# Kernel tuning notes

Measured on AMD Instinct MI355X. Metric: run time of the kernel, lower is better.

Reference implementation:

```python
import jax, jax.numpy as jnp
import numpy as np

N = 65536      # total nodes
B = 512        # graphs (equal-sized)
NPER = N // B  # 128 nodes per graph
E = 655360     # edges
F_IN = 128
K = 32         # sort-pool k
OUT = 27


def _gcn(x, row, col, dinv, W, b):
    # PyG GCNConv with added self-loops and symmetric normalization:
    xw = x @ W                                   # [N, F_out]
    coef = dinv[row] * dinv[col]                 # [E]
    agg = jax.ops.segment_sum(xw[row] * coef[:, None], col, num_segments=N)
    return agg + (dinv * dinv)[:, None] * xw + b  # self-loop term + bias


def _conv1d(x, w, b, stride):
    # x: [B, C_in, L], w: [C_out, C_in, K]
    out = jax.lax.conv_general_dilated(x, w, (stride,), 'VALID',
                                       dimension_numbers=('NCH', 'OIH', 'NCH'))
    return out + b[None, :, None]


def setup_inputs() -> dict:
    key = jax.random.key(0)
    ks = jax.random.split(key, 16)
    x = jax.random.normal(ks[0], (N, F_IN), dtype=jnp.float32)
    edge_index = jax.random.randint(ks[1], (2, E), 0, N, dtype=jnp.int32)
    batch = jnp.repeat(jnp.arange(B, dtype=jnp.int32), NPER)

    def lin(k, fi, fo):
        return jax.random.normal(k, (fi, fo), dtype=jnp.float32) / np.sqrt(fi)

    W1, b1 = lin(ks[2], F_IN, 128), jnp.zeros((128,), jnp.float32)
    W2, b2 = lin(ks[3], 128, 64), jnp.zeros((64,), jnp.float32)
    W3, b3 = lin(ks[4], 64, 32), jnp.zeros((32,), jnp.float32)
    W4, b4 = lin(ks[5], 32, 32), jnp.zeros((32,), jnp.float32)
    conv5_w = jax.random.normal(ks[6], (16, 1, 256), jnp.float32) / np.sqrt(256)
    conv5_b = jnp.zeros((16,), jnp.float32)
    conv6_w = jax.random.normal(ks[7], (32, 16, 5), jnp.float32) / np.sqrt(16 * 5)
    conv6_b = jnp.zeros((32,), jnp.float32)
    dense_w = lin(ks[8], 384, OUT)
    dense_b = jnp.zeros((OUT,), jnp.float32)
    return dict(x=x, edge_index=edge_index, batch=batch,
                W1=W1, b1=b1, W2=W2, b2=b2, W3=W3, b3=b3, W4=W4, b4=b4,
                conv5_w=conv5_w, conv5_b=conv5_b, conv6_w=conv6_w, conv6_b=conv6_b,
                dense_w=dense_w, dense_b=dense_b)


def reference(x, edge_index, batch, W1, b1, W2, b2, W3, b3, W4, b4,
              conv5_w, conv5_b, conv6_w, conv6_b, dense_w, dense_b):
    row, col = edge_index[0], edge_index[1]
    deg = jax.ops.segment_sum(jnp.ones((E,), x.dtype), col, num_segments=N) + 1.0
    dinv = jax.lax.rsqrt(deg)

    x1 = jnp.tanh(_gcn(x, row, col, dinv, W1, b1))
    x2 = jnp.tanh(_gcn(x1, row, col, dinv, W2, b2))
    x3 = jnp.tanh(_gcn(x2, row, col, dinv, W3, b3))
    x4 = jnp.tanh(_gcn(x3, row, col, dinv, W4, b4))
    h = jnp.concatenate([x1, x2, x3, x4], axis=-1)   # [N, 256]

    # SortAggregation: sort nodes within each graph by last channel (desc), take top-k.
    hg = h.reshape(B, NPER, 256)
    idx = jnp.argsort(-hg[:, :, -1], axis=1)[:, :K]                 # [B, K]
    pooled = jnp.take_along_axis(hg, idx[:, :, None], axis=1)       # [B, K, 256]
    top_k_indices = idx + (jnp.arange(B, dtype=idx.dtype) * NPER)[:, None]

    z = pooled.reshape(B, 1, K * 256)                # [B, 1, 8192]
    z = jax.nn.relu(_conv1d(z, conv5_w, conv5_b, 256))  # [B, 16, 32]
    z = jax.lax.reduce_window(z, -jnp.inf, jax.lax.max,
                              (1, 1, 2), (1, 1, 2), 'VALID')        # [B, 16, 16]
    z = jax.nn.relu(_conv1d(z, conv6_w, conv6_b, 1))  # [B, 32, 12]
    z = z.reshape(B, -1)                              # [B, 384]
    out = z @ dense_w + dense_b                       # [B, 27]
    return out, top_k_indices
```

## Files before the change

kernel.cpp:

```cpp
#include <hip/hip_runtime.h>
#include <math.h>

#define N_NODES 65536
#define N_EDGES 655360
#define N_GRAPHS 512
#define NPERG 128
#define KTOP 32
#define NOUT 27
#define OUT0_SIZE (N_GRAPHS * NOUT)
#define EPS 64

typedef unsigned int uint32;
typedef unsigned short u16;
typedef unsigned char u8;
typedef __attribute__((ext_vector_type(8))) short bf16x8;
typedef __attribute__((ext_vector_type(4))) float f32x4;
typedef __attribute__((ext_vector_type(2))) float f32x2;

__device__ __forceinline__ float blo(uint32 u) { return __uint_as_float(u << 16); }
__device__ __forceinline__ float bhi(uint32 u) { return __uint_as_float(u & 0xffff0000u); }
__device__ __forceinline__ u16 f2b(float f) {
    uint32 u = __float_as_uint(f);
    u += 0x7fffu + ((u >> 16) & 1u);
    return (u16)(u >> 16);
}
__device__ __forceinline__ uint32 pk(float a, float b) {
    return (uint32)f2b(a) | ((uint32)f2b(b) << 16);
}
__device__ __forceinline__ f32x2 fp8lo(uint32 u) { return __builtin_amdgcn_cvt_pk_f32_fp8((int)u, false); }
__device__ __forceinline__ f32x2 fp8hi(uint32 u) { return __builtin_amdgcn_cvt_pk_f32_fp8((int)u, true); }
__device__ __forceinline__ u8 f2fp8(float v) {
    return (u8)(__builtin_amdgcn_cvt_pk_fp8_f32(v, v, 0, false) & 0xff);
}


__global__ __launch_bounds__(256) void zero_kernel(int* __restrict__ cur) {
    cur[blockIdx.x * 256 + threadIdx.x] = 0;
}


template<int FI, int FO>
__device__ __forceinline__ void pack_w(const float* __restrict__ W, uint4* __restrict__ pw,
                                       int base, int nb) {
    constexpr int KC = FI / 8;
    for (int q = (blockIdx.x - base) * 256 + threadIdx.x; q < FO * KC; q += nb * 256) {
        int n = q % FO, c = q / FO;
        const float* wp = W + (size_t)(c * 8) * FO + n;
        uint4 v;
        v.x = pk(wp[0],            wp[(size_t)FO]);
        v.y = pk(wp[2*(size_t)FO], wp[3*(size_t)FO]);
        v.z = pk(wp[4*(size_t)FO], wp[5*(size_t)FO]);
        v.w = pk(wp[6*(size_t)FO], wp[7*(size_t)FO]);
        pw[n * KC + c] = v;
    }
}

__global__ __launch_bounds__(256) void prep_w(const float* __restrict__ W1, const float* __restrict__ W2,
                                              const float* __restrict__ W3, const float* __restrict__ W4,
                                              uint4* __restrict__ pw1, uint4* __restrict__ pw2,
                                              uint4* __restrict__ pw3, uint4* __restrict__ pw4) {
    int b = blockIdx.x;
    if (b < 8)       pack_w<128, 128>(W1, pw1, 0, 8);
    else if (b < 12) pack_w<128, 64>(W2, pw2, 8, 4);
    else if (b < 13) pack_w<64, 32>(W3, pw3, 12, 1);
    else             pack_w<32, 32>(W4, pw4, 13, 1);
}


__global__ __launch_bounds__(256) void fill_kernel(const int* __restrict__ erow, const int* __restrict__ ecol,
                                                   int* __restrict__ cur, u16* __restrict__ ep) {
    int e = blockIdx.x * 256 + threadIdx.x;
    int r = erow[e], d = ecol[e];
    int slot = atomicAdd(&cur[d], 1);
    if (slot < EPS) ep[(d << 6) + slot] = (u16)r;
}


__global__ __launch_bounds__(256) void dinv_kernel(const int* __restrict__ cur, float* __restrict__ dinv) {
    int i = blockIdx.x * 256 + threadIdx.x;
    dinv[i] = rsqrtf((float)cur[i] + 1.0f);
}


template<int FI, int FO>
__device__ __forceinline__ void stage_Bp(const uint4* __restrict__ pw, uint4* __restrict__ Bs) {
    constexpr int KC = FI / 8, SA = KC + 1;
    for (int q = threadIdx.x; q < FO * KC; q += 256) {
        int n = q / KC, c = q % KC;
        Bs[n * SA + c] = pw[q];
    }
}

template<int FI, int FO, bool OUT_FP8>
__device__ __forceinline__ void mfma_store(uint4* __restrict__ As, const uint4* __restrict__ Bs,
                                           uint4* __restrict__ Y, size_t rowbase,
                                           const float* __restrict__ ds) {
    constexpr int KC = FI / 8, SA = KC + 1;
    constexpr int NTILE = FO / 16;
    constexpr int CW = (NTILE >= 4) ? 4 : NTILE;
    constexpr int NTW = NTILE / CW;
    constexpr int RW = 4 / CW;
    constexpr int RS = 2 / RW;
    constexpr int KSTEPS = FI / 32;
    int t = threadIdx.x;
    int w = t >> 6, L = t & 63;
    int quad = L >> 4, m = L & 15;
    int cw = w % CW, rw = w / CW;

    const bf16x8* Asv = (const bf16x8*)As;
    const bf16x8* Bsv = (const bf16x8*)Bs;

    f32x4 acc[RS][NTW];
#pragma unroll
    for (int i = 0; i < RS; i++)
#pragma unroll
        for (int j = 0; j < NTW; j++) acc[i][j] = (f32x4)0.f;

#pragma unroll
    for (int ks = 0; ks < KSTEPS; ks++) {
        int kc = ks * 4 + quad;
        bf16x8 bfr[NTW];
#pragma unroll
        for (int j = 0; j < NTW; j++) {
            int n = (cw * NTW + j) * 16 + m;
            bfr[j] = Bsv[n * SA + kc];
        }
#pragma unroll
        for (int i = 0; i < RS; i++) {
            int r = (rw * RS + i) * 16 + m;
            bf16x8 afr = Asv[r * SA + kc];
#pragma unroll
            for (int j = 0; j < NTW; j++)
                acc[i][j] = __builtin_amdgcn_mfma_f32_16x16x32_bf16(afr, bfr[j], acc[i][j], 0, 0, 0);
        }
    }
    __syncthreads();

    if constexpr (OUT_FP8) {
        u8* outs = (u8*)As;
#pragma unroll
        for (int i = 0; i < RS; i++) {
            int rb = (rw * RS + i) * 16 + quad * 4;
#pragma unroll
            for (int j = 0; j < NTW; j++) {
                int cc = (cw * NTW + j) * 16 + m;
#pragma unroll
                for (int g2 = 0; g2 < 4; g2++)
                    outs[(rb + g2) * FO + cc] = f2fp8(acc[i][j][g2] * ds[rb + g2]);
            }
        }
    } else {
        u16* outs = (u16*)As;
#pragma unroll
        for (int i = 0; i < RS; i++) {
            int rb = (rw * RS + i) * 16 + quad * 4;
#pragma unroll
            for (int j = 0; j < NTW; j++) {
                int cc = (cw * NTW + j) * 16 + m;
#pragma unroll
                for (int g2 = 0; g2 < 4; g2++)
                    outs[(rb + g2) * FO + cc] = f2b(acc[i][j][g2] * ds[rb + g2]);
            }
        }
    }
    __syncthreads();
    constexpr int NU4 = OUT_FP8 ? (32 * FO / 16) : (32 * FO / 8);
    for (int q = t; q < NU4; q += 256)
        Y[rowbase * (NU4 / 32) + q] = ((const uint4*)As)[q];
}


__global__ __launch_bounds__(256) void gemm1_kernel(const float* __restrict__ x,
                                                    const uint4* __restrict__ pw1,
                                                    const float* __restrict__ dinv,
                                                    uint4* __restrict__ xw1) {
    constexpr int KC = 16, SA = 17;
    __shared__ __align__(16) uint4 As[32 * SA];
    __shared__ __align__(16) uint4 Bs[128 * SA];
    __shared__ float ds[32];
    int t = threadIdx.x;
    stage_Bp<128, 128>(pw1, Bs);
    size_t rowbase = (size_t)blockIdx.x * 32;
    if (t < 32) ds[t] = dinv[rowbase + t];
    for (int q = t; q < 32 * KC; q += 256) {
        int r = q / KC, c = q % KC;
        const float* xp = x + (rowbase + r) * 128 + c * 8;
        float4 v0 = *(const float4*)xp;
        float4 v1 = *(const float4*)(xp + 4);
        uint4 u;
        u.x = pk(v0.x, v0.y); u.y = pk(v0.z, v0.w);
        u.z = pk(v1.x, v1.y); u.w = pk(v1.z, v1.w);
        As[r * SA + c] = u;
    }
    __syncthreads();
    mfma_store<128, 128, true>(As, Bs, xw1, rowbase, ds);
}


template<int F>
__device__ __forceinline__ void agg_node_fp8(const uint32* __restrict__ xin1,
                                             const u16* __restrict__ ep,
                                             int n, int c4, int deg, float dn,
                                             const float* __restrict__ bias,
                                             float& r0, float& r1, float& r2, float& r3) {
    constexpr int L4 = F / 4;
    const u16* epp = ep + (n << 6);
    float a0=0.f,a1=0.f,a2=0.f,a3=0.f,b0=0.f,b1=0.f,b2=0.f,b3=0.f;
    float c0=0.f,c1=0.f,c2=0.f,c3=0.f,d0=0.f,d1=0.f,d2=0.f,d3=0.f;
    int full = deg >> 3; if (full > EPS / 8) full = EPS / 8;
    for (int b = 0; b < full; b++) {
        uint4 e8 = *(const uint4*)(epp + b * 8);
        uint32 q0=e8.x&0xffffu, q1=e8.x>>16, q2=e8.y&0xffffu, q3=e8.y>>16;
        uint32 q4=e8.z&0xffffu, q5=e8.z>>16, q6=e8.w&0xffffu, q7=e8.w>>16;
        uint32 g0=xin1[(size_t)q0*L4+c4], g1=xin1[(size_t)q1*L4+c4];
        uint32 g2=xin1[(size_t)q2*L4+c4], g3=xin1[(size_t)q3*L4+c4];
        uint32 g4=xin1[(size_t)q4*L4+c4], g5=xin1[(size_t)q5*L4+c4];
        uint32 g6=xin1[(size_t)q6*L4+c4], g7=xin1[(size_t)q7*L4+c4];
        f32x2 l, h;
        l=fp8lo(g0); h=fp8hi(g0); a0+=l.x; a1+=l.y; a2+=h.x; a3+=h.y;
        l=fp8lo(g1); h=fp8hi(g1); b0+=l.x; b1+=l.y; b2+=h.x; b3+=h.y;
        l=fp8lo(g2); h=fp8hi(g2); c0+=l.x; c1+=l.y; c2+=h.x; c3+=h.y;
        l=fp8lo(g3); h=fp8hi(g3); d0+=l.x; d1+=l.y; d2+=h.x; d3+=h.y;
        l=fp8lo(g4); h=fp8hi(g4); a0+=l.x; a1+=l.y; a2+=h.x; a3+=h.y;
        l=fp8lo(g5); h=fp8hi(g5); b0+=l.x; b1+=l.y; b2+=h.x; b3+=h.y;
        l=fp8lo(g6); h=fp8hi(g6); c0+=l.x; c1+=l.y; c2+=h.x; c3+=h.y;
        l=fp8lo(g7); h=fp8hi(g7); d0+=l.x; d1+=l.y; d2+=h.x; d3+=h.y;
    }
    int rem = (full == EPS / 8) ? 0 : (deg & 7);
    if (rem) {
        uint4 e8 = *(const uint4*)(epp + full * 8);
        uint32 q0=e8.x&0xffffu, q1=e8.x>>16, q2=e8.y&0xffffu, q3=e8.y>>16;
        uint32 q4=e8.z&0xffffu, q5=e8.z>>16, q6=e8.w&0xffffu, q7=e8.w>>16;
        uint32 g0=xin1[(size_t)q0*L4+c4], g1=xin1[(size_t)q1*L4+c4];
        uint32 g2=xin1[(size_t)q2*L4+c4], g3=xin1[(size_t)q3*L4+c4];
        uint32 g4=xin1[(size_t)q4*L4+c4], g5=xin1[(size_t)q5*L4+c4];
        uint32 g6=xin1[(size_t)q6*L4+c4], g7=xin1[(size_t)q7*L4+c4];
        g0 = (rem > 0) ? g0 : 0u; g1 = (rem > 1) ? g1 : 0u;
        g2 = (rem > 2) ? g2 : 0u; g3 = (rem > 3) ? g3 : 0u;
        g4 = (rem > 4) ? g4 : 0u; g5 = (rem > 5) ? g5 : 0u;
        g6 = (rem > 6) ? g6 : 0u; g7 = (rem > 7) ? g7 : 0u;
        f32x2 l, h;
        l=fp8lo(g0); h=fp8hi(g0); a0+=l.x; a1+=l.y; a2+=h.x; a3+=h.y;
        l=fp8lo(g1); h=fp8hi(g1); b0+=l.x; b1+=l.y; b2+=h.x; b3+=h.y;
        l=fp8lo(g2); h=fp8hi(g2); c0+=l.x; c1+=l.y; c2+=h.x; c3+=h.y;
        l=fp8lo(g3); h=fp8hi(g3); d0+=l.x; d1+=l.y; d2+=h.x; d3+=h.y;
        l=fp8lo(g4); h=fp8hi(g4); a0+=l.x; a1+=l.y; a2+=h.x; a3+=h.y;
        l=fp8lo(g5); h=fp8hi(g5); b0+=l.x; b1+=l.y; b2+=h.x; b3+=h.y;
        l=fp8lo(g6); h=fp8hi(g6); c0+=l.x; c1+=l.y; c2+=h.x; c3+=h.y;
        l=fp8lo(g7); h=fp8hi(g7); d0+=l.x; d1+=l.y; d2+=h.x; d3+=h.y;
    }
    uint32 sv = xin1[(size_t)n * L4 + c4];
    f32x2 sl = fp8lo(sv), sh = fp8hi(sv);
    r0 = dn * ((a0+b0+c0+d0) + sl.x) + bias[4*c4+0];
    r1 = dn * ((a1+b1+c1+d1) + sl.y) + bias[4*c4+1];
    r2 = dn * ((a2+b2+c2+d2) + sh.x) + bias[4*c4+2];
    r3 = dn * ((a3+b3+c3+d3) + sh.y) + bias[4*c4+3];
}

template<int F>
__device__ __forceinline__ void agg_node_bf16(const uint2* __restrict__ xin2,
                                              const u16* __restrict__ ep,
                                              int n, int c4, int deg, float dn,
                                              const float* __restrict__ bias,
                                              float& r0, float& r1, float& r2, float& r3) {
    constexpr int L4 = F / 4;
    const u16* epp = ep + (n << 6);
    float a0=0.f,a1=0.f,a2=0.f,a3=0.f,b0=0.f,b1=0.f,b2=0.f,b3=0.f;
    float c0=0.f,c1=0.f,c2=0.f,c3=0.f,d0=0.f,d1=0.f,d2=0.f,d3=0.f;
    int full = deg >> 3; if (full > EPS / 8) full = EPS / 8;
    for (int b = 0; b < full; b++) {
        uint4 e8 = *(const uint4*)(epp + b * 8);
        uint32 q0=e8.x&0xffffu, q1=e8.x>>16, q2=e8.y&0xffffu, q3=e8.y>>16;
        uint32 q4=e8.z&0xffffu, q5=e8.z>>16, q6=e8.w&0xffffu, q7=e8.w>>16;
        uint2 g0=xin2[(size_t)q0*L4+c4], g1=xin2[(size_t)q1*L4+c4];
        uint2 g2=xin2[(size_t)q2*L4+c4], g3=xin2[(size_t)q3*L4+c4];
        uint2 g4=xin2[(size_t)q4*L4+c4], g5=xin2[(size_t)q5*L4+c4];
        uint2 g6=xin2[(size_t)q6*L4+c4], g7=xin2[(size_t)q7*L4+c4];
        a0+=blo(g0.x); a1+=bhi(g0.x); a2+=blo(g0.y); a3+=bhi(g0.y);
        b0+=blo(g1.x); b1+=bhi(g1.x); b2+=blo(g1.y); b3+=bhi(g1.y);
        c0+=blo(g2.x); c1+=bhi(g2.x); c2+=blo(g2.y); c3+=bhi(g2.y);
        d0+=blo(g3.x); d1+=bhi(g3.x); d2+=blo(g3.y); d3+=bhi(g3.y);
        a0+=blo(g4.x); a1+=bhi(g4.x); a2+=blo(g4.y); a3+=bhi(g4.y);
        b0+=blo(g5.x); b1+=bhi(g5.x); b2+=blo(g5.y); b3+=bhi(g5.y);
        c0+=blo(g6.x); c1+=bhi(g6.x); c2+=blo(g6.y); c3+=bhi(g6.y);
        d0+=blo(g7.x); d1+=bhi(g7.x); d2+=blo(g7.y); d3+=bhi(g7.y);
    }
    int rem = (full == EPS / 8) ? 0 : (deg & 7);
    if (rem) {
        uint4 e8 = *(const uint4*)(epp + full * 8);
        uint32 q0=e8.x&0xffffu, q1=e8.x>>16, q2=e8.y&0xffffu, q3=e8.y>>16;
        uint32 q4=e8.z&0xffffu, q5=e8.z>>16, q6=e8.w&0xffffu, q7=e8.w>>16;
        uint2 g0=xin2[(size_t)q0*L4+c4], g1=xin2[(size_t)q1*L4+c4];
        uint2 g2=xin2[(size_t)q2*L4+c4], g3=xin2[(size_t)q3*L4+c4];
        uint2 g4=xin2[(size_t)q4*L4+c4], g5=xin2[(size_t)q5*L4+c4];
        uint2 g6=xin2[(size_t)q6*L4+c4], g7=xin2[(size_t)q7*L4+c4];
        g0.x=(rem>0)?g0.x:0u; g0.y=(rem>0)?g0.y:0u;
        g1.x=(rem>1)?g1.x:0u; g1.y=(rem>1)?g1.y:0u;
        g2.x=(rem>2)?g2.x:0u; g2.y=(rem>2)?g2.y:0u;
        g3.x=(rem>3)?g3.x:0u; g3.y=(rem>3)?g3.y:0u;
        g4.x=(rem>4)?g4.x:0u; g4.y=(rem>4)?g4.y:0u;
        g5.x=(rem>5)?g5.x:0u; g5.y=(rem>5)?g5.y:0u;
        g6.x=(rem>6)?g6.x:0u; g6.y=(rem>6)?g6.y:0u;
        g7.x=(rem>7)?g7.x:0u; g7.y=(rem>7)?g7.y:0u;
        a0+=blo(g0.x); a1+=bhi(g0.x); a2+=blo(g0.y); a3+=bhi(g0.y);
        b0+=blo(g1.x); b1+=bhi(g1.x); b2+=blo(g1.y); b3+=bhi(g1.y);
        c0+=blo(g2.x); c1+=bhi(g2.x); c2+=blo(g2.y); c3+=bhi(g2.y);
        d0+=blo(g3.x); d1+=bhi(g3.x); d2+=blo(g3.y); d3+=bhi(g3.y);
        a0+=blo(g4.x); a1+=bhi(g4.x); a2+=blo(g4.y); a3+=bhi(g4.y);
        b0+=blo(g5.x); b1+=bhi(g5.x); b2+=blo(g5.y); b3+=bhi(g5.y);
        c0+=blo(g6.x); c1+=bhi(g6.x); c2+=blo(g6.y); c3+=bhi(g6.y);
        d0+=blo(g7.x); d1+=bhi(g7.x); d2+=blo(g7.y); d3+=bhi(g7.y);
    }
    uint2 sv = xin2[(size_t)n * L4 + c4];
    r0 = dn * ((a0+b0+c0+d0) + blo(sv.x)) + bias[4*c4+0];
    r1 = dn * ((a1+b1+c1+d1) + bhi(sv.x)) + bias[4*c4+1];
    r2 = dn * ((a2+b2+c2+d2) + blo(sv.y)) + bias[4*c4+2];
    r3 = dn * ((a3+b3+c3+d3) + bhi(sv.y)) + bias[4*c4+3];
}


template<int F, int FO, bool IN_FP8>
__global__ __launch_bounds__(256, 6) void agg_gemm(const uint32* __restrict__ xin,
                                                   const int* __restrict__ cur,
                                                   const u16* __restrict__ ep,
                                                   const float* __restrict__ dinv,
                                                   const float* __restrict__ bias,
                                                   const uint4* __restrict__ pw,
                                                   uint32* __restrict__ hc, int co2,
                                                   uint4* __restrict__ xout) {
    constexpr int KC = F / 8, SA = KC + 1;
    constexpr int L4 = F / 4;
    constexpr int NPP = 256 / L4;
    __shared__ __align__(16) uint4 As[32 * SA];
    __shared__ __align__(16) uint4 Bs[FO * SA];
    __shared__ float ds[32];
    int t = threadIdx.x;
    int rowbase = blockIdx.x * 32;
    stage_Bp<F, FO>(pw, Bs);
    if (t < 32) ds[t] = dinv[rowbase + t];
    __syncthreads();

    uint2* As2 = (uint2*)As;
    uint2* hc2 = (uint2*)hc;
    int c4 = t % L4;
    int nsub = t / L4;
#pragma unroll
    for (int pass = 0; pass < 32 / NPP; pass++) {
        int nl = pass * NPP + nsub;
        int n = rowbase + nl;
        int deg = cur[n];
        float dn = ds[nl];
        float r0, r1, r2, r3;
        if constexpr (IN_FP8)
            agg_node_fp8<F>(xin, ep, n, c4, deg, dn, bias, r0, r1, r2, r3);
        else
            agg_node_bf16<F>((const uint2*)xin, ep, n, c4, deg, dn, bias, r0, r1, r2, r3);
        uint2 pr;
        pr.x = pk(tanhf(r0), tanhf(r1));
        pr.y = pk(tanhf(r2), tanhf(r3));
        hc2[(size_t)n * 64 + co2 + c4] = pr;
        As2[nl * (SA * 2) + c4] = pr;
    }
    __syncthreads();
    mfma_store<F, FO, false>(As, Bs, xout, (size_t)rowbase, ds);
}


__global__ __launch_bounds__(256) void agg_last(const uint32* __restrict__ xin,
                                                const int* __restrict__ cur,
                                                const u16* __restrict__ ep,
                                                const float* __restrict__ dinv,
                                                const float* __restrict__ b4,
                                                uint32* __restrict__ hc) {
    int t = threadIdx.x;
    int c4 = t & 7, nsub = t >> 3;
    int n = blockIdx.x * 32 + nsub;
    int deg = cur[n];
    float dn = dinv[n];
    float r0, r1, r2, r3;
    agg_node_bf16<32>((const uint2*)xin, ep, n, c4, deg, dn, b4, r0, r1, r2, r3);
    uint2 pr;
    pr.x = pk(tanhf(r0), tanhf(r1));
    pr.y = pk(tanhf(r2), tanhf(r3));
    ((uint2*)hc)[(size_t)n * 64 + 56 + c4] = pr;
}


__global__ __launch_bounds__(256) void final_kernel(const uint32* __restrict__ hc,
                                                    const float* __restrict__ w5, const float* __restrict__ b5,
                                                    const float* __restrict__ w6, const float* __restrict__ b6,
                                                    const float* __restrict__ dw, const float* __restrict__ db,
                                                    float* __restrict__ out) {
    __shared__ float skey[128];
    __shared__ int   sidx[128];
    __shared__ uint32 ph[32 * 133];
    __shared__ float w5s[4096];
    __shared__ float z5[16 * 33];
    __shared__ float ms[16 * 17];
    __shared__ float z6[384];
    int g = blockIdx.x, t = threadIdx.x;

    for (int q = t; q < 4096; q += 256) w5s[q] = w5[q];
    if (t < 128) { skey[t] = bhi(hc[(size_t)(g * NPERG + t) * 128 + 127]); sidx[t] = t; }
    __syncthreads();

    for (int sz = 2; sz <= 128; sz <<= 1) {
        for (int stride = sz >> 1; stride > 0; stride >>= 1) {
            if (t < 64) {
                int i = ((t & ~(stride - 1)) << 1) | (t & (stride - 1));
                int j = i | stride;
                float ki = skey[i], kj = skey[j];
                int ii = sidx[i], ij = sidx[j];
                bool desc = ((i & sz) == 0);
                bool ibef = (ki > kj) || (ki == kj && ii < ij);
                if (desc != ibef) { skey[i] = kj; skey[j] = ki; sidx[i] = ij; sidx[j] = ii; }
            }
            __syncthreads();
        }
    }

    if (t < KTOP) out[OUT0_SIZE + g * KTOP + t] = (float)(g * NPERG + sidx[t]);

    {
        const uint4* hcv = (const uint4*)hc;
        int rsub = t >> 5, cell = t & 31;
#pragma unroll
        for (int p = 0; p < 4; p++) {
            int r2 = p * 8 + rsub;
            int node = g * NPERG + sidx[r2];
            uint4 v = hcv[(size_t)node * 32 + cell];
            uint32* dst = &ph[r2 * 133 + cell * 4];
            dst[0] = v.x; dst[1] = v.y; dst[2] = v.z; dst[3] = v.w;
        }
    }
    __syncthreads();

    {
        int o = t >> 5, l = t & 31;
        float a0 = 0.f, a1 = 0.f;
#pragma unroll 4
        for (int j2 = 0; j2 < 128; j2++) {
            uint32 u = ph[l * 133 + j2];
            float p0 = blo(u), p1 = bhi(u);
            a0 += p0 * w5s[o * 256 + 2 * j2]       + p1 * w5s[o * 256 + 2 * j2 + 1];
            a1 += p0 * w5s[(o + 8) * 256 + 2 * j2] + p1 * w5s[(o + 8) * 256 + 2 * j2 + 1];
        }
        z5[o * 33 + l]       = fmaxf(a0 + b5[o], 0.f);
        z5[(o + 8) * 33 + l] = fmaxf(a1 + b5[o + 8], 0.f);
    }
    __syncthreads();

    {
        int o = t >> 4, p = t & 15;
        ms[o * 17 + p] = fmaxf(z5[o * 33 + 2 * p], z5[o * 33 + 2 * p + 1]);
    }
    __syncthreads();

    for (int q = t; q < 384; q += 256) {
        int o2 = q / 12, tt = q % 12;
        float a = b6[o2];
        for (int o = 0; o < 16; o++) {
#pragma unroll
            for (int k = 0; k < 5; k++)
                a += w6[(o2 * 16 + o) * 5 + k] * ms[o * 17 + tt + k];
        }
        z6[q] = fmaxf(a, 0.f);
    }
    __syncthreads();

    if (t < NOUT) {
        float a = db[t];
        for (int i = 0; i < 384; i++) a += z6[i] * dw[i * NOUT + t];
        out[g * NOUT + t] = a;
    }
}


extern "C" void kernel_launch(void* const* d_in, const int* in_sizes, int n_in,
                              void* d_out, int out_size, void* d_ws, size_t ws_size,
                              hipStream_t stream) {
    const float* x    = (const float*)d_in[0];
    const int*   edge = (const int*)d_in[1];
    const int*   erow = edge;
    const int*   ecol = edge + N_EDGES;
    const float* W1 = (const float*)d_in[3];  const float* b1 = (const float*)d_in[4];
    const float* W2 = (const float*)d_in[5];  const float* b2 = (const float*)d_in[6];
    const float* W3 = (const float*)d_in[7];  const float* b3 = (const float*)d_in[8];
    const float* W4 = (const float*)d_in[9];  const float* b4 = (const float*)d_in[10];
    const float* w5 = (const float*)d_in[11]; const float* b5 = (const float*)d_in[12];
    const float* w6 = (const float*)d_in[13]; const float* b6 = (const float*)d_in[14];
    const float* dw = (const float*)d_in[15]; const float* db = (const float*)d_in[16];
    float* out = (float*)d_out;

    char* wsb = (char*)d_ws;
    size_t off = 0;
    auto alloc = [&](size_t bytes) -> void* {
        void* p = wsb + off;
        off = (off + bytes + 255) & ~(size_t)255;
        return p;
    };
    int*    cur  = (int*)   alloc((size_t)N_NODES * 4);
    float*  dinv = (float*) alloc((size_t)N_NODES * 4);
    u16*    ep   = (u16*)   alloc((size_t)N_NODES * EPS * 2);
    uint32* xwA  = (uint32*)alloc((size_t)N_NODES * 32 * 4);
    uint32* xwB  = (uint32*)alloc((size_t)N_NODES * 32 * 4);
    uint32* hc   = (uint32*)alloc((size_t)N_NODES * 128 * 4);
    uint4*  pw1  = (uint4*) alloc(2048 * 16);
    uint4*  pw2  = (uint4*) alloc(1024 * 16);
    uint4*  pw3  = (uint4*) alloc(256 * 16);
    uint4*  pw4  = (uint4*) alloc(128 * 16);
    (void)ws_size; (void)in_sizes; (void)n_in; (void)out_size;

    zero_kernel<<<N_NODES / 256, 256, 0, stream>>>(cur);
    prep_w<<<14, 256, 0, stream>>>(W1, W2, W3, W4, pw1, pw2, pw3, pw4);
    fill_kernel<<<N_EDGES / 256, 256, 0, stream>>>(erow, ecol, cur, ep);
    dinv_kernel<<<N_NODES / 256, 256, 0, stream>>>(cur, dinv);
    gemm1_kernel<<<N_NODES / 32, 256, 0, stream>>>(x, pw1, dinv, (uint4*)xwA);
    agg_gemm<128, 64, true><<<N_NODES / 32, 256, 0, stream>>>(xwA, cur, ep, dinv, b1, pw2, hc, 0, (uint4*)xwB);
    agg_gemm<64, 32, false><<<N_NODES / 32, 256, 0, stream>>>(xwB, cur, ep, dinv, b2, pw3, hc, 32, (uint4*)xwA);
    agg_gemm<32, 32, false><<<N_NODES / 32, 256, 0, stream>>>(xwA, cur, ep, dinv, b3, pw4, hc, 48, (uint4*)xwB);
    agg_last<<<N_NODES / 32, 256, 0, stream>>>(xwB, cur, ep, dinv, b4, hc);
    final_kernel<<<N_GRAPHS, 256, 0, stream>>>(hc, w5, b5, w6, b6, dw, db, out);
}
```

Before: 246.4 us.

## Unroll neighbor gather to fixed 32 edges with masking and store layer-2 input as fp8

Merges the fp8 and bf16 aggregation helpers into one template. The new helper always issues 32 masked gathers up front, so many loads are in flight together instead of running a variable-length loop of 8. Edges beyond 32 go through a scalar tail loop. Layer 1's GEMM output is now written in fp8, so layer 2 reads its gathered features as fp8, halving that gather's bytes at some precision cost. Launch bounds drop from 6 to 4 waves per SIMD, giving more registers in exchange for lower occupancy, and low-degree nodes now issue wasted masked loads to node 0.

```diff
diff --git a/kernel.cpp b/kernel.cpp
--- a/kernel.cpp
+++ b/kernel.cpp
@@ -197,130 +197,86 @@
 }
 
 
-template<int F>
-__device__ __forceinline__ void agg_node_fp8(const uint32* __restrict__ xin1,
-                                             const u16* __restrict__ ep,
-                                             int n, int c4, int deg, float dn,
-                                             const float* __restrict__ bias,
-                                             float& r0, float& r1, float& r2, float& r3) {
+template<int F, bool FP8>
+__device__ __forceinline__ void agg_node(const void* __restrict__ xin,
+                                         const u16* __restrict__ ep,
+                                         int n, int c4, int deg, float dn,
+                                         const float* __restrict__ bias,
+                                         float& r0, float& r1, float& r2, float& r3) {
     constexpr int L4 = F / 4;
+    const uint32* x1 = (const uint32*)xin;
+    const uint2*  x2 = (const uint2*)xin;
     const u16* epp = ep + (n << 6);
-    float a0=0.f,a1=0.f,a2=0.f,a3=0.f,b0=0.f,b1=0.f,b2=0.f,b3=0.f;
-    float c0=0.f,c1=0.f,c2=0.f,c3=0.f,d0=0.f,d1=0.f,d2=0.f,d3=0.f;
-    int full = deg >> 3; if (full > EPS / 8) full = EPS / 8;
-    for (int b = 0; b < full; b++) {
-        uint4 e8 = *(const uint4*)(epp + b * 8);
-        uint32 q0=e8.x&0xffffu, q1=e8.x>>16, q2=e8.y&0xffffu, q3=e8.y>>16;
-        uint32 q4=e8.z&0xffffu, q5=e8.z>>16, q6=e8.w&0xffffu, q7=e8.w>>16;
-        uint32 g0=xin1[(size_t)q0*L4+c4], g1=xin1[(size_t)q1*L4+c4];
-        uint32 g2=xin1[(size_t)q2*L4+c4], g3=xin1[(size_t)q3*L4+c4];
-        uint32 g4=xin1[(size_t)q4*L4+c4], g5=xin1[(size_t)q5*L4+c4];
-        uint32 g6=xin1[(size_t)q6*L4+c4], g7=xin1[(size_t)q7*L4+c4];
-        f32x2 l, h;
-        l=fp8lo(g0); h=fp8hi(g0); a0+=l.x; a1+=l.y; a2+=h.x; a3+=h.y;
-        l=fp8lo(g1); h=fp8hi(g1); b0+=l.x; b1+=l.y; b2+=h.x; b3+=h.y;
-        l=fp8lo(g2); h=fp8hi(g2); c0+=l.x; c1+=l.y; c2+=h.x; c3+=h.y;
-        l=fp8lo(g3); h=fp8hi(g3); d0+=l.x; d1+=l.y; d2+=h.x; d3+=h.y;
-        l=fp8lo(g4); h=fp8hi(g4); a0+=l.x; a1+=l.y; a2+=h.x; a3+=h.y;
-        l=fp8lo(g5); h=fp8hi(g5); b0+=l.x; b1+=l.y; b2+=h.x; b3+=h.y;
-        l=fp8lo(g6); h=fp8hi(g6); c0+=l.x; c1+=l.y; c2+=h.x; c3+=h.y;
-        l=fp8lo(g7); h=fp8hi(g7); d0+=l.x; d1+=l.y; d2+=h.x; d3+=h.y;
-    }
-    int rem = (full == EPS / 8) ? 0 : (deg & 7);
-    if (rem) {
-        uint4 e8 = *(const uint4*)(epp + full * 8);
-        uint32 q0=e8.x&0xffffu, q1=e8.x>>16, q2=e8.y&0xffffu, q3=e8.y>>16;
-        uint32 q4=e8.z&0xffffu, q5=e8.z>>16, q6=e8.w&0xffffu, q7=e8.w>>16;
-        uint32 g0=xin1[(size_t)q0*L4+c4], g1=xin1[(size_t)q1*L4+c4];
-        uint32 g2=xin1[(size_t)q2*L4+c4], g3=xin1[(size_t)q3*L4+c4];
-        uint32 g4=xin1[(size_t)q4*L4+c4], g5=xin1[(size_t)q5*L4+c4];
-        uint32 g6=xin1[(size_t)q6*L4+c4], g7=xin1[(size_t)q7*L4+c4];
-        g0 = (rem > 0) ? g0 : 0u; g1 = (rem > 1) ? g1 : 0u;
-        g2 = (rem > 2) ? g2 : 0u; g3 = (rem > 3) ? g3 : 0u;
-        g4 = (rem > 4) ? g4 : 0u; g5 = (rem > 5) ? g5 : 0u;
-        g6 = (rem > 6) ? g6 : 0u; g7 = (rem > 7) ? g7 : 0u;
-        f32x2 l, h;
-        l=fp8lo(g0); h=fp8hi(g0); a0+=l.x; a1+=l.y; a2+=h.x; a3+=h.y;
-        l=fp8lo(g1); h=fp8hi(g1); b0+=l.x; b1+=l.y; b2+=h.x; b3+=h.y;
-        l=fp8lo(g2); h=fp8hi(g2); c0+=l.x; c1+=l.y; c2+=h.x; c3+=h.y;
-        l=fp8lo(g3); h=fp8hi(g3); d0+=l.x; d1+=l.y; d2+=h.x; d3+=h.y;
-        l=fp8lo(g4); h=fp8hi(g4); a0+=l.x; a1+=l.y; a2+=h.x; a3+=h.y;
-        l=fp8lo(g5); h=fp8hi(g5); b0+=l.x; b1+=l.y; b2+=h.x; b3+=h.y;
-        l=fp8lo(g6); h=fp8hi(g6); c0+=l.x; c1+=l.y; c2+=h.x; c3+=h.y;
-        l=fp8lo(g7); h=fp8hi(g7); d0+=l.x; d1+=l.y; d2+=h.x; d3+=h.y;
-    }
-    uint32 sv = xin1[(size_t)n * L4 + c4];
-    f32x2 sl = fp8lo(sv), sh = fp8hi(sv);
-    r0 = dn * ((a0+b0+c0+d0) + sl.x) + bias[4*c4+0];
-    r1 = dn * ((a1+b1+c1+d1) + sl.y) + bias[4*c4+1];
-    r2 = dn * ((a2+b2+c2+d2) + sh.x) + bias[4*c4+2];
-    r3 = dn * ((a3+b3+c3+d3) + sh.y) + bias[4*c4+3];
-}
-
-template<int F>
-__device__ __forceinline__ void agg_node_bf16(const uint2* __restrict__ xin2,
-                                              const u16* __restrict__ ep,
-                                              int n, int c4, int deg, float dn,
-                                              const float* __restrict__ bias,
-                                              float& r0, float& r1, float& r2, float& r3) {
-    constexpr int L4 = F / 4;
-    const u16* epp = ep + (n << 6);
-    float a0=0.f,a1=0.f,a2=0.f,a3=0.f,b0=0.f,b1=0.f,b2=0.f,b3=0.f;
-    float c0=0.f,c1=0.f,c2=0.f,c3=0.f,d0=0.f,d1=0.f,d2=0.f,d3=0.f;
-    int full = deg >> 3; if (full > EPS / 8) full = EPS / 8;
-    for (int b = 0; b < full; b++) {
-        uint4 e8 = *(const uint4*)(epp + b * 8);
-        uint32 q0=e8.x&0xffffu, q1=e8.x>>16, q2=e8.y&0xffffu, q3=e8.y>>16;
-        uint32 q4=e8.z&0xffffu, q5=e8.z>>16, q6=e8.w&0xffffu, q7=e8.w>>16;
-        uint2 g0=xin2[(size_t)q0*L4+c4], g1=xin2[(size_t)q1*L4+c4];
-        uint2 g2=xin2[(size_t)q2*L4+c4], g3=xin2[(size_t)q3*L4+c4];
-        uint2 g4=xin2[(size_t)q4*L4+c4], g5=xin2[(size_t)q5*L4+c4];
-        uint2 g6=xin2[(size_t)q6*L4+c4], g7=xin2[(size_t)q7*L4+c4];
-        a0+=blo(g0.x); a1+=bhi(g0.x); a2+=blo(g0.y); a3+=bhi(g0.y);
-        b0+=blo(g1.x); b1+=bhi(g1.x); b2+=blo(g1.y); b3+=bhi(g1.y);
-        c0+=blo(g2.x); c1+=bhi(g2.x); c2+=blo(g2.y); c3+=bhi(g2.y);
-        d0+=blo(g3.x); d1+=bhi(g3.x); d2+=blo(g3.y); d3+=bhi(g3.y);
-        a0+=blo(g4.x); a1+=bhi(g4.x); a2+=blo(g4.y); a3+=bhi(g4.y);
-        b0+=blo(g5.x); b1+=bhi(g5.x); b2+=blo(g5.y); b3+=bhi(g5.y);
-        c0+=blo(g6.x); c1+=bhi(g6.x); c2+=blo(g6.y); c3+=bhi(g6.y);
-        d0+=blo(g7.x); d1+=bhi(g7.x); d2+=blo(g7.y); d3+=bhi(g7.y);
-    }
-    int rem = (full == EPS / 8) ? 0 : (deg & 7);
-    if (rem) {
-        uint4 e8 = *(const uint4*)(epp + full * 8);
-        uint32 q0=e8.x&0xffffu, q1=e8.x>>16, q2=e8.y&0xffffu, q3=e8.y>>16;
-        uint32 q4=e8.z&0xffffu, q5=e8.z>>16, q6=e8.w&0xffffu, q7=e8.w>>16;
-        uint2 g0=xin2[(size_t)q0*L4+c4], g1=xin2[(size_t)q1*L4+c4];
-        uint2 g2=xin2[(size_t)q2*L4+c4], g3=xin2[(size_t)q3*L4+c4];
-        uint2 g4=xin2[(size_t)q4*L4+c4], g5=xin2[(size_t)q5*L4+c4];
-        uint2 g6=xin2[(size_t)q6*L4+c4], g7=xin2[(size_t)q7*L4+c4];
-        g0.x=(rem>0)?g0.x:0u; g0.y=(rem>0)?g0.y:0u;
-        g1.x=(rem>1)?g1.x:0u; g1.y=(rem>1)?g1.y:0u;
-        g2.x=(rem>2)?g2.x:0u; g2.y=(rem>2)?g2.y:0u;
-        g3.x=(rem>3)?g3.x:0u; g3.y=(rem>3)?g3.y:0u;
-        g4.x=(rem>4)?g4.x:0u; g4.y=(rem>4)?g4.y:0u;
-        g5.x=(rem>5)?g5.x:0u; g5.y=(rem>5)?g5.y:0u;
-        g6.x=(rem>6)?g6.x:0u; g6.y=(rem>6)?g6.y:0u;
-        g7.x=(rem>7)?g7.x:0u; g7.y=(rem>7)?g7.y:0u;
-        a0+=blo(g0.x); a1+=bhi(g0.x); a2+=blo(g0.y); a3+=bhi(g0.y);
-        b0+=blo(g1.x); b1+=bhi(g1.x); b2+=blo(g1.y); b3+=bhi(g1.y);
-        c0+=blo(g2.x); c1+=bhi(g2.x); c2+=blo(g2.y); c3+=bhi(g2.y);
-        d0+=blo(g3.x); d1+=bhi(g3.x); d2+=blo(g3.y); d3+=bhi(g3.y);
-        a0+=blo(g4.x); a1+=bhi(g4.x); a2+=blo(g4.y); a3+=bhi(g4.y);
-        b0+=blo(g5.x); b1+=bhi(g5.x); b2+=blo(g5.y); b3+=bhi(g5.y);
-        c0+=blo(g6.x); c1+=bhi(g6.x); c2+=blo(g6.y); c3+=bhi(g6.y);
-        d0+=blo(g7.x); d1+=bhi(g7.x); d2+=blo(g7.y); d3+=bhi(g7.y);
-    }
-    uint2 sv = xin2[(size_t)n * L4 + c4];
-    r0 = dn * ((a0+b0+c0+d0) + blo(sv.x)) + bias[4*c4+0];
-    r1 = dn * ((a1+b1+c1+d1) + bhi(sv.x)) + bias[4*c4+1];
-    r2 = dn * ((a2+b2+c2+d2) + blo(sv.y)) + bias[4*c4+2];
-    r3 = dn * ((a3+b3+c3+d3) + bhi(sv.y)) + bias[4*c4+3];
-}
-
-
-template<int F, int FO, bool IN_FP8>
-__global__ __launch_bounds__(256, 6) void agg_gemm(const uint32* __restrict__ xin,
+    float ac[4][4];
+#pragma unroll
+    for (int i = 0; i < 4; i++)
+#pragma unroll
+        for (int j = 0; j < 4; j++) ac[i][j] = 0.f;
+
+    uint4 eb[4];
+#pragma unroll
+    for (int b = 0; b < 4; b++) eb[b] = *(const uint4*)(epp + b * 8);
+
+#pragma unroll
+    for (int b = 0; b < 4; b++) {
+        uint32 qq[8] = { eb[b].x & 0xffffu, eb[b].x >> 16, eb[b].y & 0xffffu, eb[b].y >> 16,
+                         eb[b].z & 0xffffu, eb[b].z >> 16, eb[b].w & 0xffffu, eb[b].w >> 16 };
+#pragma unroll
+        for (int j = 0; j < 8; j++) {
+            bool ok = (b * 8 + j) < deg;
+            uint32 src = ok ? qq[j] : 0u;
+            if constexpr (FP8) {
+                uint32 g = x1[(size_t)src * L4 + c4];
+                g = ok ? g : 0u;
+                f32x2 l = fp8lo(g), h = fp8hi(g);
+                ac[j & 3][0] += l.x; ac[j & 3][1] += l.y;
+                ac[j & 3][2] += h.x; ac[j & 3][3] += h.y;
+            } else {
+                uint2 g = x2[(size_t)src * L4 + c4];
+                uint32 gx = ok ? g.x : 0u, gy = ok ? g.y : 0u;
+                ac[j & 3][0] += blo(gx); ac[j & 3][1] += bhi(gx);
+                ac[j & 3][2] += blo(gy); ac[j & 3][3] += bhi(gy);
+            }
+        }
+    }
+    if (deg > 32) {
+        int hi = min(deg, EPS);
+        for (int p = 32; p < hi; p++) {
+            uint32 src = epp[p];
+            if constexpr (FP8) {
+                uint32 g = x1[(size_t)src * L4 + c4];
+                f32x2 l = fp8lo(g), h = fp8hi(g);
+                ac[0][0] += l.x; ac[0][1] += l.y; ac[0][2] += h.x; ac[0][3] += h.y;
+            } else {
+                uint2 g = x2[(size_t)src * L4 + c4];
+                ac[0][0] += blo(g.x); ac[0][1] += bhi(g.x);
+                ac[0][2] += blo(g.y); ac[0][3] += bhi(g.y);
+            }
+        }
+    }
+    float s0 = (ac[0][0] + ac[1][0]) + (ac[2][0] + ac[3][0]);
+    float s1 = (ac[0][1] + ac[1][1]) + (ac[2][1] + ac[3][1]);
+    float s2 = (ac[0][2] + ac[1][2]) + (ac[2][2] + ac[3][2]);
+    float s3 = (ac[0][3] + ac[1][3]) + (ac[2][3] + ac[3][3]);
+    if constexpr (FP8) {
+        uint32 sv = x1[(size_t)n * L4 + c4];
+        f32x2 sl = fp8lo(sv), sh = fp8hi(sv);
+        r0 = dn * (s0 + sl.x) + bias[4 * c4 + 0];
+        r1 = dn * (s1 + sl.y) + bias[4 * c4 + 1];
+        r2 = dn * (s2 + sh.x) + bias[4 * c4 + 2];
+        r3 = dn * (s3 + sh.y) + bias[4 * c4 + 3];
+    } else {
+        uint2 sv = x2[(size_t)n * L4 + c4];
+        r0 = dn * (s0 + blo(sv.x)) + bias[4 * c4 + 0];
+        r1 = dn * (s1 + bhi(sv.x)) + bias[4 * c4 + 1];
+        r2 = dn * (s2 + blo(sv.y)) + bias[4 * c4 + 2];
+        r3 = dn * (s3 + bhi(sv.y)) + bias[4 * c4 + 3];
+    }
+}
+
+
+template<int F, int FO, bool IN_FP8, bool OUT_FP8>
+__global__ __launch_bounds__(256, 4) void agg_gemm(const uint32* __restrict__ xin,
                                                    const int* __restrict__ cur,
                                                    const u16* __restrict__ ep,
                                                    const float* __restrict__ dinv,
@@ -351,10 +307,7 @@
         int deg = cur[n];
         float dn = ds[nl];
         float r0, r1, r2, r3;
-        if constexpr (IN_FP8)
-            agg_node_fp8<F>(xin, ep, n, c4, deg, dn, bias, r0, r1, r2, r3);
-        else
-            agg_node_bf16<F>((const uint2*)xin, ep, n, c4, deg, dn, bias, r0, r1, r2, r3);
+        agg_node<F, IN_FP8>(xin, ep, n, c4, deg, dn, bias, r0, r1, r2, r3);
         uint2 pr;
         pr.x = pk(tanhf(r0), tanhf(r1));
         pr.y = pk(tanhf(r2), tanhf(r3));
@@ -362,23 +315,23 @@
         As2[nl * (SA * 2) + c4] = pr;
     }
     __syncthreads();
-    mfma_store<F, FO, false>(As, Bs, xout, (size_t)rowbase, ds);
-}
-
-
-__global__ __launch_bounds__(256) void agg_last(const uint32* __restrict__ xin,
-                                                const int* __restrict__ cur,
-                                                const u16* __restrict__ ep,
-                                                const float* __restrict__ dinv,
-                                                const float* __restrict__ b4,
-                                                uint32* __restrict__ hc) {
+    mfma_store<F, FO, OUT_FP8>(As, Bs, xout, (size_t)rowbase, ds);
+}
+
+
+__global__ __launch_bounds__(256, 4) void agg_last(const uint32* __restrict__ xin,
+                                                   const int* __restrict__ cur,
+                                                   const u16* __restrict__ ep,
+                                                   const float* __restrict__ dinv,
+                                                   const float* __restrict__ b4,
+                                                   uint32* __restrict__ hc) {
     int t = threadIdx.x;
     int c4 = t & 7, nsub = t >> 3;
     int n = blockIdx.x * 32 + nsub;
     int deg = cur[n];
     float dn = dinv[n];
     float r0, r1, r2, r3;
-    agg_node_bf16<32>((const uint2*)xin, ep, n, c4, deg, dn, b4, r0, r1, r2, r3);
+    agg_node<32, false>(xin, ep, n, c4, deg, dn, b4, r0, r1, r2, r3);
     uint2 pr;
     pr.x = pk(tanhf(r0), tanhf(r1));
     pr.y = pk(tanhf(r2), tanhf(r3));
@@ -516,9 +469,9 @@
     fill_kernel<<<N_EDGES / 256, 256, 0, stream>>>(erow, ecol, cur, ep);
     dinv_kernel<<<N_NODES / 256, 256, 0, stream>>>(cur, dinv);
     gemm1_kernel<<<N_NODES / 32, 256, 0, stream>>>(x, pw1, dinv, (uint4*)xwA);
-    agg_gemm<128, 64, true><<<N_NODES / 32, 256, 0, stream>>>(xwA, cur, ep, dinv, b1, pw2, hc, 0, (uint4*)xwB);
-    agg_gemm<64, 32, false><<<N_NODES / 32, 256, 0, stream>>>(xwB, cur, ep, dinv, b2, pw3, hc, 32, (uint4*)xwA);
-    agg_gemm<32, 32, false><<<N_NODES / 32, 256, 0, stream>>>(xwA, cur, ep, dinv, b3, pw4, hc, 48, (uint4*)xwB);
+    agg_gemm<128, 64, true, true><<<N_NODES / 32, 256, 0, stream>>>(xwA, cur, ep, dinv, b1, pw2, hc, 0, (uint4*)xwB);
+    agg_gemm<64, 32, true, false><<<N_NODES / 32, 256, 0, stream>>>(xwB, cur, ep, dinv, b2, pw3, hc, 32, (uint4*)xwA);
+    agg_gemm<32, 32, false, false><<<N_NODES / 32, 256, 0, stream>>>(xwA, cur, ep, dinv, b3, pw4, hc, 48, (uint4*)xwB);
     agg_last<<<N_NODES / 32, 256, 0, stream>>>(xwB, cur, ep, dinv, b4, hc);
     final_kernel<<<N_GRAPHS, 256, 0, stream>>>(hc, w5, b5, w6, b6, dw, db, out);
 }
```

New measurement: 253.4 us. +2.8%, slower.
